# Kernel tuning notes

Hardware: AMD Instinct MI355X
Metric: run time of the kernel (lower is better)

## Reference

```python
import jax, jax.numpy as jnp
import numpy as np

H = 16        # heads
DH = 64       # dim_head
DM = 1024     # query_dim = context_dim
INNER = H * DH


def setup_inputs() -> dict:
    key = jax.random.key(0)
    ks = jax.random.split(key, 5)
    s = 0.02
    queries = jax.random.normal(ks[0], (2, 2048, DM), dtype=jnp.float32)
    Wq = jax.random.normal(ks[1], (DM, INNER), dtype=jnp.float32) * s
    Wkv = jax.random.normal(ks[2], (DM, 2 * INNER), dtype=jnp.float32) * s
    Wo = jax.random.normal(ks[3], (INNER, DM), dtype=jnp.float32) * s
    bo = jax.random.normal(ks[4], (DM,), dtype=jnp.float32) * s
    return {"queries": queries, "Wq": Wq, "Wkv": Wkv, "Wo": Wo, "bo": bo}


def reference(queries, Wq, Wkv, Wo, bo):
    b, n, _ = queries.shape
    scale = DH ** -0.5
    q = queries @ Wq                       # [b, n, inner]
    kv = queries @ Wkv                     # self-attention: context = queries
    k, v = jnp.split(kv, 2, axis=-1)
    # b n (h d) -> b h n d
    split_heads = lambda t: t.reshape(b, n, H, DH).transpose(0, 2, 1, 3)
    q, k, v = map(split_heads, (q, k, v))
    sim = jnp.einsum('bhid,bhjd->bhij', q, k) * scale
    attn = jax.nn.softmax(sim, axis=-1)    # dropout is identity (p=0 / eval)
    out = jnp.einsum('bhij,bhjd->bhid', attn, v)
    out = out.transpose(0, 2, 1, 3).reshape(b, n, INNER)
    return out @ Wo + bo
```

## Files before the change

### kernel.cpp

```cpp
#include <hip/hip_runtime.h>
#include <math.h>
#include <stdint.h>

typedef _Float16 half8v __attribute__((ext_vector_type(8)));
typedef _Float16 half4v __attribute__((ext_vector_type(4)));
typedef _Float16 half2v __attribute__((ext_vector_type(2)));
typedef __fp16 fp16x2 __attribute__((ext_vector_type(2)));
typedef float floatx4 __attribute__((ext_vector_type(4)));

#define MFMA16(a, b, c) __builtin_amdgcn_mfma_f32_16x16x32_f16(a, b, c, 0, 0, 0)

#define QSCALE 0.18033688011112f

__device__ __forceinline__ void gld_lds16(const void* g, void* l) {
  __builtin_amdgcn_global_load_lds(
      (const __attribute__((address_space(1))) uint32_t*)(uintptr_t)g,
      (__attribute__((address_space(3))) uint32_t*)(uintptr_t)l, 16, 0, 0);
}

__device__ __forceinline__ half2v pk16(float a, float b) {
  fp16x2 t = __builtin_amdgcn_cvt_pkrtz(a, b);
  return __builtin_bit_cast(half2v, t);
}

__device__ __forceinline__ int swz(int row, int blk) {
  return row * 64 + ((blk ^ (row & 7)) << 3);
}

__device__ __forceinline__ int vswz(int row, int blk) {
  return row * 32 + ((blk ^ ((row >> 1) & 3)) << 3);
}

__device__ __forceinline__ int gswz(int row, int blk) {
  return row * 32 + ((blk ^ ((row >> 1) & 3)) << 3);
}

__global__ __launch_bounds__(256) void prep(
    const float* __restrict__ X, const float* __restrict__ Wq,
    const float* __restrict__ Wkv, const float* __restrict__ Wo,
    _Float16* __restrict__ X16, _Float16* __restrict__ WqkvT,
    _Float16* __restrict__ WoT)
{
  __shared__ alignas(16) _Float16 Tt[64 * 68];
  const int bid = blockIdx.x;
  if (bid < 2048) {
    size_t gid = (size_t)bid * 256 + threadIdx.x;
    const float4* src = (const float4*)(X) + gid * 2;
    float4 a = src[0], b = src[1];
    half8v h;
    h[0]=(_Float16)a.x; h[1]=(_Float16)a.y; h[2]=(_Float16)a.z; h[3]=(_Float16)a.w;
    h[4]=(_Float16)b.x; h[5]=(_Float16)b.y; h[6]=(_Float16)b.z; h[7]=(_Float16)b.w;
    *((half8v*)X16 + gid) = h;
    return;
  }
  int b = bid - 2048;
  const float* src; _Float16* dst; int N, tk, tn;
  if (b < 256)      { src = Wq;  dst = WqkvT;                 N = 1024; tk = b & 15;        tn = b >> 4; }
  else if (b < 768) { src = Wkv; dst = WqkvT + (size_t)1024 * 1024; N = 2048; tk = (b - 256) & 15; tn = (b - 256) >> 4; }
  else              { src = Wo;  dst = WoT;                   N = 1024; tk = (b - 768) & 15; tn = (b - 768) >> 4; }

  const int t = threadIdx.x;
  {
    int kg = t >> 4, ng = t & 15;
    const float* sp = src + (size_t)(tk * 64 + kg * 4) * N + tn * 64 + ng * 4;
    float4 r0 = *(const float4*)(sp);
    float4 r1 = *(const float4*)(sp + N);
    float4 r2 = *(const float4*)(sp + 2 * N);
    float4 r3 = *(const float4*)(sp + 3 * N);
    half4v h;
    h[0]=(_Float16)r0.x; h[1]=(_Float16)r1.x; h[2]=(_Float16)r2.x; h[3]=(_Float16)r3.x;
    *(half4v*)&Tt[(ng * 4 + 0) * 68 + kg * 4] = h;
    h[0]=(_Float16)r0.y; h[1]=(_Float16)r1.y; h[2]=(_Float16)r2.y; h[3]=(_Float16)r3.y;
    *(half4v*)&Tt[(ng * 4 + 1) * 68 + kg * 4] = h;
    h[0]=(_Float16)r0.z; h[1]=(_Float16)r1.z; h[2]=(_Float16)r2.z; h[3]=(_Float16)r3.z;
    *(half4v*)&Tt[(ng * 4 + 2) * 68 + kg * 4] = h;
    h[0]=(_Float16)r0.w; h[1]=(_Float16)r1.w; h[2]=(_Float16)r2.w; h[3]=(_Float16)r3.w;
    *(half4v*)&Tt[(ng * 4 + 3) * 68 + kg * 4] = h;
  }
  __syncthreads();
  #pragma unroll
  for (int i = 0; i < 2; i++) {
    int idx = t + i * 256;
    int nl = idx >> 3, k8 = (idx & 7) * 8;
    half8v v = *(half8v*)&Tt[nl * 68 + k8];
    *(half8v*)(dst + (size_t)(tn * 64 + nl) * 1024 + tk * 64 + k8) = v;
  }
}

__global__ __launch_bounds__(256) void qkv_gemm(
    const _Float16* __restrict__ X16, const _Float16* __restrict__ WqkvT,
    _Float16* __restrict__ q_ws, _Float16* __restrict__ k_ws,
    _Float16* __restrict__ vT_ws)
{
  constexpr int K = 1024;
  __shared__ alignas(16) _Float16 Tt[128 * 136];
  _Float16* As = Tt;
  _Float16* Bs = Tt + 4096;

  const int m0 = blockIdx.x * 128;
  const int n0 = blockIdx.y * 128;

  const int tid  = threadIdx.x;
  const int wave = tid >> 6, lane = tid & 63;
  const int qd = lane >> 4, l15 = lane & 15;
  const int wr = (wave >> 1) * 64, wc = (wave & 1) * 64;
  const int r0i = tid >> 2;
  const int cbs = (((tid & 3) ^ ((r0i >> 1) & 3))) * 8;

  floatx4 acc[4][4] = {};

  for (int k0 = 0; k0 < K; k0 += 32) {
    gld_lds16(X16 + (size_t)(m0 + r0i) * K + k0 + cbs, &As[tid * 8]);
    gld_lds16(X16 + (size_t)(m0 + 64 + r0i) * K + k0 + cbs, &As[(tid + 256) * 8]);
    gld_lds16(WqkvT + (size_t)(n0 + r0i) * K + k0 + cbs, &Bs[tid * 8]);
    gld_lds16(WqkvT + (size_t)(n0 + 64 + r0i) * K + k0 + cbs, &Bs[(tid + 256) * 8]);
    __syncthreads();
    half8v a[4], b[4];
    #pragma unroll
    for (int it = 0; it < 4; it++)
      a[it] = *(half8v*)&As[gswz(wr + it * 16 + l15, qd)];
    #pragma unroll
    for (int jt = 0; jt < 4; jt++)
      b[jt] = *(half8v*)&Bs[gswz(wc + jt * 16 + l15, qd)];
    #pragma unroll
    for (int it = 0; it < 4; it++)
      #pragma unroll
      for (int jt = 0; jt < 4; jt++)
        acc[it][jt] = MFMA16(a[it], b[jt], acc[it][jt]);
    __syncthreads();
  }

  if (n0 < 2048) {
    #pragma unroll
    for (int it = 0; it < 4; it++) {
      #pragma unroll
      for (int jt = 0; jt < 4; jt++) {
        #pragma unroll
        for (int r = 0; r < 4; r++) {
          int m = m0 + wr + it * 16 + qd * 4 + r;
          int n = n0 + wc + jt * 16 + l15;
          float val = acc[it][jt][r];
          int bb = m >> 11, nn = m & 2047;
          if (n0 < 1024) {
            int h = n >> 6, d = n & 63;
            q_ws[(((size_t)bb * 16 + h) * 2048 + nn) * 64 + d] = (_Float16)(val * QSCALE);
          } else {
            int c = n - 1024, h = c >> 6, d = c & 63;
            k_ws[(((size_t)bb * 16 + h) * 2048 + nn) * 64 + d] = (_Float16)val;
          }
        }
      }
    }
  } else {
    #pragma unroll
    for (int it = 0; it < 4; it++) {
      #pragma unroll
      for (int jt = 0; jt < 4; jt++) {
        #pragma unroll
        for (int r = 0; r < 4; r++) {
          int ml = wr + it * 16 + qd * 4 + r;
          int nl = wc + jt * 16 + l15;
          Tt[nl * 136 + ml] = (_Float16)acc[it][jt][r];
        }
      }
    }
    __syncthreads();
    int row = tid >> 1;
    int mh  = (tid & 1) * 64;
    int c   = (n0 - 2048) + row;
    int bb  = m0 >> 11;
    int nnb = (m0 & 2047) + mh;
    _Float16* dstp =
        vT_ws + (((size_t)bb * 16 + (c >> 6)) * 64 + (c & 63)) * 2048 + nnb;
    #pragma unroll
    for (int i = 0; i < 8; i++)
      *(half8v*)(dstp + i * 8) = *(half8v*)&Tt[row * 136 + mh + i * 8];
  }
}

__global__ __launch_bounds__(256, 3) void attn_kernel(
    const _Float16* __restrict__ q_ws, const _Float16* __restrict__ k_ws,
    const _Float16* __restrict__ vT_ws, _Float16* __restrict__ aout)
{
  constexpr int N = 2048;
  __shared__ alignas(16) char smem[50176];
  _Float16* Kbase = (_Float16*)smem;
  _Float16* Vbase = (_Float16*)(smem + 16384);
  _Float16* PQ    = (_Float16*)(smem + 32768);

  const int id = blockIdx.x;
  const int bh = ((id >> 8) << 3) | (id & 7);
  const int qt = (id >> 3) & 31;

  const _Float16* Qp = q_ws + (size_t)bh * N * 64;
  const _Float16* Kp = k_ws + (size_t)bh * N * 64;
  const _Float16* Vp = vT_ws + (size_t)bh * 64 * N;

  const int tid = threadIdx.x, wave = tid >> 6, lane = tid & 63;
  const int qd = lane >> 4, l15 = lane & 15;
  const int q0 = qt * 64;
  const int wkv = wave * 32;

  _Float16* Ks = Kbase + wave * 2048;
  _Float16* Vs = Vbase + wave * 2048;
  _Float16* Ps = PQ + wave * 2048;

  const int krr = lane >> 3, kcb = (lane & 7) ^ krr;
  const int vrr = lane >> 2, vcb = (lane & 3) ^ ((lane >> 3) & 3);
  const int kwr = (krr * 64 + (kcb << 3));

  auto stage_v = [&](int il) {
    const _Float16* src = Vp + wkv + il * 128;
    #pragma unroll
    for (int j = 0; j < 4; j++)
      gld_lds16(src + (size_t)(j * 16 + vrr) * N + vcb * 8,
                Vs + (j * 64 + lane) * 8);
  };

  #pragma unroll
  for (int i = 0; i < 2; i++) {
    int idx = tid + i * 256;
    int r = idx >> 3, cb = (idx ^ r) & 7;
    gld_lds16(Qp + (size_t)(q0 + r) * 64 + cb * 8, PQ + idx * 8);
  }
  {
    const _Float16* src = Kp + (size_t)wkv * 64;
    #pragma unroll
    for (int j = 0; j < 4; j++)
      gld_lds16(src + (size_t)(j * 8 + krr) * 64 + kcb * 8,
                Ks + (j * 64 + lane) * 8);
  }
  stage_v(0);
  const _Float16* Kw = Kp + (size_t)wkv * 64;
  half8v kr0, kr1, kr2, kr3;
  {
    const _Float16* nb = Kw + (size_t)1 * 8192 + lane * 8;
    kr0 = *(const half8v*)(nb);
    kr1 = *(const half8v*)(nb + 512);
    kr2 = *(const half8v*)(nb + 1024);
    kr3 = *(const half8v*)(nb + 1536);
  }

  asm volatile("s_waitcnt vmcnt(8)" ::: "memory");
  __builtin_amdgcn_s_barrier();
  __builtin_amdgcn_sched_barrier(0);

  half8v qf[4][2];
  #pragma unroll
  for (int m = 0; m < 4; m++)
    #pragma unroll
    for (int ks = 0; ks < 2; ks++)
      qf[m][ks] = *(half8v*)&PQ[swz(m * 16 + l15, ks * 4 + qd)];

  asm volatile("s_waitcnt lgkmcnt(0)" ::: "memory");
  __builtin_amdgcn_s_barrier();
  __builtin_amdgcn_sched_barrier(0);

  floatx4 o[4][4] = {};
  float lsum[4] = {};

  for (int i = 0; i < 16; ++i) {
    floatx4 s[2][4] = {};
    #pragma unroll
    for (int ks = 0; ks < 2; ks++) {
      half8v kf0 = *(half8v*)&Ks[swz(l15, ks * 4 + qd)];
      half8v kf1 = *(half8v*)&Ks[swz(16 + l15, ks * 4 + qd)];
      __builtin_amdgcn_s_setprio(1);
      #pragma unroll
      for (int m = 0; m < 4; m++) {
        s[0][m] = MFMA16(kf0, qf[m][ks], s[0][m]);
        s[1][m] = MFMA16(kf1, qf[m][ks], s[1][m]);
      }
      __builtin_amdgcn_s_setprio(0);
    }

    #pragma unroll
    for (int m = 0; m < 4; m++)
      #pragma unroll
      for (int nt = 0; nt < 2; nt++) {
        float p0 = __builtin_amdgcn_exp2f(s[nt][m][0]);
        float p1 = __builtin_amdgcn_exp2f(s[nt][m][1]);
        float p2 = __builtin_amdgcn_exp2f(s[nt][m][2]);
        float p3 = __builtin_amdgcn_exp2f(s[nt][m][3]);
        lsum[m] += (p0 + p1) + (p2 + p3);
        half2v h01 = pk16(p0, p1);
        half2v h23 = pk16(p2, p3);
        half4v pk;
        pk[0] = h01[0]; pk[1] = h01[1]; pk[2] = h23[0]; pk[3] = h23[1];
        *(half4v*)&Ps[vswz(m * 16 + l15, 2 * nt + (qd >> 1)) + (qd & 1) * 4] = pk;
      }

    if (i < 15) asm volatile("s_waitcnt vmcnt(4)" ::: "memory");
    else        asm volatile("s_waitcnt vmcnt(0)" ::: "memory");
    __builtin_amdgcn_sched_barrier(0);

    half8v pf[4], vf[4];
    #pragma unroll
    for (int m = 0; m < 4; m++)
      pf[m] = *(half8v*)&Ps[vswz(m * 16 + l15, qd)];
    #pragma unroll
    for (int dt = 0; dt < 4; dt++)
      vf[dt] = *(half8v*)&Vs[vswz(dt * 16 + l15, qd)];

    asm volatile("s_waitcnt lgkmcnt(0)" ::: "memory");
    __builtin_amdgcn_sched_barrier(0);

    if (i < 15) {
      _Float16* wr = Ks + kwr;
      *(half8v*)(wr)        = kr0;
      *(half8v*)(wr + 512)  = kr1;
      *(half8v*)(wr + 1024) = kr2;
      *(half8v*)(wr + 1536) = kr3;
    }
    __builtin_amdgcn_sched_barrier(0);

    if (i < 15) stage_v(i + 1);
    if (i < 14) {
      const _Float16* nb = Kw + (size_t)(i + 2) * 8192 + lane * 8;
      kr0 = *(const half8v*)(nb);
      kr1 = *(const half8v*)(nb + 512);
      kr2 = *(const half8v*)(nb + 1024);
      kr3 = *(const half8v*)(nb + 1536);
    }
    __builtin_amdgcn_sched_barrier(0);

    __builtin_amdgcn_s_setprio(1);
    #pragma unroll
    for (int m = 0; m < 4; m++)
      #pragma unroll
      for (int dt = 0; dt < 4; dt++)
        o[m][dt] = MFMA16(pf[m], vf[dt], o[m][dt]);
    __builtin_amdgcn_s_setprio(0);
  }

  #pragma unroll
  for (int m = 0; m < 4; m++) {
    lsum[m] += __shfl_xor(lsum[m], 16);
    lsum[m] += __shfl_xor(lsum[m], 32);
  }

  __syncthreads();
  float* sc = (float*)smem;
  float* ls = (float*)(smem + 49152);
  #pragma unroll
  for (int m = 0; m < 4; m++)
    if (qd == 0) ls[wave * 64 + m * 16 + l15] = lsum[m];

  const int bb = bh >> 4, hh = bh & 15;
  #pragma unroll
  for (int pass = 0; pass < 2; pass++) {
    float* my = sc + wave * 2176;
    #pragma unroll
    for (int mm = 0; mm < 2; mm++) {
      int m = pass * 2 + mm;
      #pragma unroll
      for (int dt = 0; dt < 4; dt++)
        #pragma unroll
        for (int r = 0; r < 4; r++)
          my[(mm * 16 + qd * 4 + r) * 68 + dt * 16 + l15] = o[m][dt][r];
    }
    __syncthreads();
    {
      int r = tid >> 3, c0 = (tid & 7) * 8;
      int row = pass * 32 + r;
      float lsv = ls[row] + ls[64 + row] + ls[128 + row] + ls[192 + row];
      float inv = 1.0f / lsv;
      float acc8[8] = {};
      #pragma unroll
      for (int w = 0; w < 4; w++) {
        const float* p = sc + w * 2176 + r * 68 + c0;
        floatx4 a = *(const floatx4*)(p);
        floatx4 b = *(const floatx4*)(p + 4);
        acc8[0] += a[0]; acc8[1] += a[1]; acc8[2] += a[2]; acc8[3] += a[3];
        acc8[4] += b[0]; acc8[5] += b[1]; acc8[6] += b[2]; acc8[7] += b[3];
      }
      _Float16 hv[8];
      #pragma unroll
      for (int j = 0; j < 4; j++) {
        half2v h = pk16(acc8[2 * j] * inv, acc8[2 * j + 1] * inv);
        hv[2 * j] = h[0]; hv[2 * j + 1] = h[1];
      }
      _Float16* dst =
          aout + ((size_t)(bb * 2048 + q0 + row)) * 1024 + hh * 64 + c0;
      *(half8v*)dst = *(half8v*)hv;
    }
    if (pass == 0) __syncthreads();
  }
}

__global__ __launch_bounds__(256) void out_gemm(
    const _Float16* __restrict__ A, const _Float16* __restrict__ WoT,
    const float* __restrict__ bo, float* __restrict__ Out)
{
  constexpr int K = 1024;
  __shared__ alignas(16) _Float16 As[64 * 32];
  __shared__ alignas(16) _Float16 Bs[128 * 32];

  const int m0 = blockIdx.x * 64;
  const int n0 = blockIdx.y * 128;
  const int tid = threadIdx.x;
  const int wave = tid >> 6, lane = tid & 63;
  const int qd = lane >> 4, l15 = lane & 15;
  const int wr = (wave >> 1) * 32, wc = (wave & 1) * 64;
  const int r0i = tid >> 2;
  const int cbs = (((tid & 3) ^ ((r0i >> 1) & 3))) * 8;

  floatx4 acc[2][4] = {};

  for (int k0 = 0; k0 < K; k0 += 32) {
    gld_lds16(A + (size_t)(m0 + r0i) * K + k0 + cbs, &As[tid * 8]);
    gld_lds16(WoT + (size_t)(n0 + r0i) * K + k0 + cbs, &Bs[tid * 8]);
    gld_lds16(WoT + (size_t)(n0 + 64 + r0i) * K + k0 + cbs, &Bs[(tid + 256) * 8]);
    __syncthreads();
    half8v a[2], b[4];
    #pragma unroll
    for (int it = 0; it < 2; it++)
      a[it] = *(half8v*)&As[gswz(wr + it * 16 + l15, qd)];
    #pragma unroll
    for (int jt = 0; jt < 4; jt++)
      b[jt] = *(half8v*)&Bs[gswz(wc + jt * 16 + l15, qd)];
    #pragma unroll
    for (int it = 0; it < 2; it++)
      #pragma unroll
      for (int jt = 0; jt < 4; jt++)
        acc[it][jt] = MFMA16(a[it], b[jt], acc[it][jt]);
    __syncthreads();
  }

  #pragma unroll
  for (int it = 0; it < 2; it++) {
    #pragma unroll
    for (int jt = 0; jt < 4; jt++) {
      int n = n0 + wc + jt * 16 + l15;
      float bias = bo[n];
      #pragma unroll
      for (int r = 0; r < 4; r++) {
        int m = m0 + wr + it * 16 + qd * 4 + r;
        Out[(size_t)m * 1024 + n] = acc[it][jt][r] + bias;
      }
    }
  }
}

extern "C" void kernel_launch(void* const* d_in, const int* in_sizes, int n_in,
                              void* d_out, int out_size, void* d_ws, size_t ws_size,
                              hipStream_t stream) {
  const float* X   = (const float*)d_in[0];
  const float* Wq  = (const float*)d_in[1];
  const float* Wkv = (const float*)d_in[2];
  const float* Wo  = (const float*)d_in[3];
  const float* bo  = (const float*)d_in[4];
  float* out = (float*)d_out;

  const size_t M4 = (size_t)4 * 1024 * 1024;
  _Float16* q_ws   = (_Float16*)d_ws;
  _Float16* k_ws   = q_ws + M4;
  _Float16* vT_ws  = k_ws + M4;
  _Float16* X16    = vT_ws + M4;
  _Float16* WqkvT  = X16 + M4;
  _Float16* WoT    = WqkvT + (size_t)3 * 1024 * 1024;
  _Float16* aout   = X16;

  prep<<<3072, 256, 0, stream>>>(X, Wq, Wkv, Wo, X16, WqkvT, WoT);
  qkv_gemm<<<dim3(32, 24), 256, 0, stream>>>(X16, WqkvT, q_ws, k_ws, vT_ws);
  attn_kernel<<<1024, 256, 0, stream>>>(q_ws, k_ws, vT_ws, aout);
  out_gemm<<<dim3(64, 8), 256, 0, stream>>>(aout, WoT, bo, out);
}
```

Baseline: 201.9 us.

## Double GEMM K-tile depth, stream K via direct LDS loads, compute row sums with MFMA

Both projection GEMMs now stage a K-slab of 64 per iteration instead of 32, using an 8-block XOR swizzle. This halves the number of barrier pairs per tile and issues more MFMAs per sync. In attention, K tiles are prefetched with global-to-LDS async loads instead of being staged through registers and written back. Softmax row sums are also accumulated by an MFMA against a ones vector, which removes the per-element adds and cross-lane shuffles but adds extra MFMA work per iteration.

```diff
diff --git a/kernel.cpp b/kernel.cpp
--- a/kernel.cpp
+++ b/kernel.cpp
@@ -28,10 +28,6 @@
 }
 
 __device__ __forceinline__ int vswz(int row, int blk) {
-  return row * 32 + ((blk ^ ((row >> 1) & 3)) << 3);
-}
-
-__device__ __forceinline__ int gswz(int row, int blk) {
   return row * 32 + ((blk ^ ((row >> 1) & 3)) << 3);
 }
 
@@ -95,7 +91,7 @@
   constexpr int K = 1024;
   __shared__ alignas(16) _Float16 Tt[128 * 136];
   _Float16* As = Tt;
-  _Float16* Bs = Tt + 4096;
+  _Float16* Bs = Tt + 8192;
 
   const int m0 = blockIdx.x * 128;
   const int n0 = blockIdx.y * 128;
@@ -104,29 +100,38 @@
   const int wave = tid >> 6, lane = tid & 63;
   const int qd = lane >> 4, l15 = lane & 15;
   const int wr = (wave >> 1) * 64, wc = (wave & 1) * 64;
-  const int r0i = tid >> 2;
-  const int cbs = (((tid & 3) ^ ((r0i >> 1) & 3))) * 8;
 
   floatx4 acc[4][4] = {};
 
-  for (int k0 = 0; k0 < K; k0 += 32) {
-    gld_lds16(X16 + (size_t)(m0 + r0i) * K + k0 + cbs, &As[tid * 8]);
-    gld_lds16(X16 + (size_t)(m0 + 64 + r0i) * K + k0 + cbs, &As[(tid + 256) * 8]);
-    gld_lds16(WqkvT + (size_t)(n0 + r0i) * K + k0 + cbs, &Bs[tid * 8]);
-    gld_lds16(WqkvT + (size_t)(n0 + 64 + r0i) * K + k0 + cbs, &Bs[(tid + 256) * 8]);
-    __syncthreads();
-    half8v a[4], b[4];
-    #pragma unroll
-    for (int it = 0; it < 4; it++)
-      a[it] = *(half8v*)&As[gswz(wr + it * 16 + l15, qd)];
-    #pragma unroll
-    for (int jt = 0; jt < 4; jt++)
-      b[jt] = *(half8v*)&Bs[gswz(wc + jt * 16 + l15, qd)];
-    #pragma unroll
-    for (int it = 0; it < 4; it++)
+  for (int k0 = 0; k0 < K; k0 += 64) {
+    #pragma unroll
+    for (int i = 0; i < 4; i++) {
+      int idx = tid + i * 256;
+      int r = idx >> 3, cb = (idx ^ r) & 7;
+      gld_lds16(X16 + (size_t)(m0 + r) * K + k0 + cb * 8, &As[idx * 8]);
+    }
+    #pragma unroll
+    for (int i = 0; i < 4; i++) {
+      int idx = tid + i * 256;
+      int r = idx >> 3, cb = (idx ^ r) & 7;
+      gld_lds16(WqkvT + (size_t)(n0 + r) * K + k0 + cb * 8, &Bs[idx * 8]);
+    }
+    __syncthreads();
+    #pragma unroll
+    for (int ks = 0; ks < 2; ks++) {
+      half8v a[4], b[4];
+      #pragma unroll
+      for (int it = 0; it < 4; it++)
+        a[it] = *(half8v*)&As[swz(wr + it * 16 + l15, ks * 4 + qd)];
       #pragma unroll
       for (int jt = 0; jt < 4; jt++)
-        acc[it][jt] = MFMA16(a[it], b[jt], acc[it][jt]);
+        b[jt] = *(half8v*)&Bs[swz(wc + jt * 16 + l15, ks * 4 + qd)];
+      #pragma unroll
+      for (int it = 0; it < 4; it++)
+        #pragma unroll
+        for (int jt = 0; jt < 4; jt++)
+          acc[it][jt] = MFMA16(a[it], b[jt], acc[it][jt]);
+    }
     __syncthreads();
   }
 
@@ -207,8 +212,14 @@
 
   const int krr = lane >> 3, kcb = (lane & 7) ^ krr;
   const int vrr = lane >> 2, vcb = (lane & 3) ^ ((lane >> 3) & 3);
-  const int kwr = (krr * 64 + (kcb << 3));
-
+
+  auto stage_k = [&](int il) {
+    const _Float16* src = Kp + (size_t)(wkv + il * 128) * 64;
+    #pragma unroll
+    for (int j = 0; j < 4; j++)
+      gld_lds16(src + (size_t)(j * 8 + krr) * 64 + kcb * 8,
+                Ks + (j * 64 + lane) * 8);
+  };
   auto stage_v = [&](int il) {
     const _Float16* src = Vp + wkv + il * 128;
     #pragma unroll
@@ -223,23 +234,8 @@
     int r = idx >> 3, cb = (idx ^ r) & 7;
     gld_lds16(Qp + (size_t)(q0 + r) * 64 + cb * 8, PQ + idx * 8);
   }
-  {
-    const _Float16* src = Kp + (size_t)wkv * 64;
-    #pragma unroll
-    for (int j = 0; j < 4; j++)
-      gld_lds16(src + (size_t)(j * 8 + krr) * 64 + kcb * 8,
-                Ks + (j * 64 + lane) * 8);
-  }
+  stage_k(0);
   stage_v(0);
-  const _Float16* Kw = Kp + (size_t)wkv * 64;
-  half8v kr0, kr1, kr2, kr3;
-  {
-    const _Float16* nb = Kw + (size_t)1 * 8192 + lane * 8;
-    kr0 = *(const half8v*)(nb);
-    kr1 = *(const half8v*)(nb + 512);
-    kr2 = *(const half8v*)(nb + 1024);
-    kr3 = *(const half8v*)(nb + 1536);
-  }
 
   asm volatile("s_waitcnt vmcnt(8)" ::: "memory");
   __builtin_amdgcn_s_barrier();
@@ -256,23 +252,36 @@
   __builtin_amdgcn_s_barrier();
   __builtin_amdgcn_sched_barrier(0);
 
+  const half8v ones = {(_Float16)1, (_Float16)1, (_Float16)1, (_Float16)1,
+                       (_Float16)1, (_Float16)1, (_Float16)1, (_Float16)1};
   floatx4 o[4][4] = {};
-  float lsum[4] = {};
+  floatx4 ol[4] = {};
 
   for (int i = 0; i < 16; ++i) {
+    asm volatile("s_waitcnt vmcnt(4)" ::: "memory");
+    __builtin_amdgcn_sched_barrier(0);
+
+    half8v kf[2][2];
+    #pragma unroll
+    for (int ks = 0; ks < 2; ks++) {
+      kf[ks][0] = *(half8v*)&Ks[swz(l15, ks * 4 + qd)];
+      kf[ks][1] = *(half8v*)&Ks[swz(16 + l15, ks * 4 + qd)];
+    }
+    asm volatile("s_waitcnt lgkmcnt(0)" ::: "memory");
+    __builtin_amdgcn_sched_barrier(0);
+    if (i < 15) stage_k(i + 1);
+    __builtin_amdgcn_sched_barrier(0);
+
     floatx4 s[2][4] = {};
-    #pragma unroll
-    for (int ks = 0; ks < 2; ks++) {
-      half8v kf0 = *(half8v*)&Ks[swz(l15, ks * 4 + qd)];
-      half8v kf1 = *(half8v*)&Ks[swz(16 + l15, ks * 4 + qd)];
-      __builtin_amdgcn_s_setprio(1);
+    __builtin_amdgcn_s_setprio(1);
+    #pragma unroll
+    for (int ks = 0; ks < 2; ks++)
       #pragma unroll
       for (int m = 0; m < 4; m++) {
-        s[0][m] = MFMA16(kf0, qf[m][ks], s[0][m]);
-        s[1][m] = MFMA16(kf1, qf[m][ks], s[1][m]);
-      }
-      __builtin_amdgcn_s_setprio(0);
-    }
+        s[0][m] = MFMA16(kf[ks][0], qf[m][ks], s[0][m]);
+        s[1][m] = MFMA16(kf[ks][1], qf[m][ks], s[1][m]);
+      }
+    __builtin_amdgcn_s_setprio(0);
 
     #pragma unroll
     for (int m = 0; m < 4; m++)
@@ -282,7 +291,6 @@
         float p1 = __builtin_amdgcn_exp2f(s[nt][m][1]);
         float p2 = __builtin_amdgcn_exp2f(s[nt][m][2]);
         float p3 = __builtin_amdgcn_exp2f(s[nt][m][3]);
-        lsum[m] += (p0 + p1) + (p2 + p3);
         half2v h01 = pk16(p0, p1);
         half2v h23 = pk16(p2, p3);
         half4v pk;
@@ -294,49 +302,29 @@
     else        asm volatile("s_waitcnt vmcnt(0)" ::: "memory");
     __builtin_amdgcn_sched_barrier(0);
 
-    half8v pf[4], vf[4];
+    half8v pf[4], vfr[4];
     #pragma unroll
     for (int m = 0; m < 4; m++)
       pf[m] = *(half8v*)&Ps[vswz(m * 16 + l15, qd)];
     #pragma unroll
     for (int dt = 0; dt < 4; dt++)
-      vf[dt] = *(half8v*)&Vs[vswz(dt * 16 + l15, qd)];
+      vfr[dt] = *(half8v*)&Vs[vswz(dt * 16 + l15, qd)];
 
     asm volatile("s_waitcnt lgkmcnt(0)" ::: "memory");
     __builtin_amdgcn_sched_barrier(0);
-
-    if (i < 15) {
-      _Float16* wr = Ks + kwr;
-      *(half8v*)(wr)        = kr0;
-      *(half8v*)(wr + 512)  = kr1;
-      *(half8v*)(wr + 1024) = kr2;
-      *(half8v*)(wr + 1536) = kr3;
-    }
-    __builtin_amdgcn_sched_barrier(0);
-
     if (i < 15) stage_v(i + 1);
-    if (i < 14) {
-      const _Float16* nb = Kw + (size_t)(i + 2) * 8192 + lane * 8;
-      kr0 = *(const half8v*)(nb);
-      kr1 = *(const half8v*)(nb + 512);
-      kr2 = *(const half8v*)(nb + 1024);
-      kr3 = *(const half8v*)(nb + 1536);
-    }
     __builtin_amdgcn_sched_barrier(0);
 
     __builtin_amdgcn_s_setprio(1);
     #pragma unroll
     for (int m = 0; m < 4; m++)
+      ol[m] = MFMA16(pf[m], ones, ol[m]);
+    #pragma unroll
+    for (int m = 0; m < 4; m++)
       #pragma unroll
       for (int dt = 0; dt < 4; dt++)
-        o[m][dt] = MFMA16(pf[m], vf[dt], o[m][dt]);
+        o[m][dt] = MFMA16(pf[m], vfr[dt], o[m][dt]);
     __builtin_amdgcn_s_setprio(0);
-  }
-
-  #pragma unroll
-  for (int m = 0; m < 4; m++) {
-    lsum[m] += __shfl_xor(lsum[m], 16);
-    lsum[m] += __shfl_xor(lsum[m], 32);
   }
 
   __syncthreads();
@@ -344,7 +332,9 @@
   float* ls = (float*)(smem + 49152);
   #pragma unroll
   for (int m = 0; m < 4; m++)
-    if (qd == 0) ls[wave * 64 + m * 16 + l15] = lsum[m];
+    #pragma unroll
+    for (int r = 0; r < 4; r++)
+      ls[wave * 64 + m * 16 + qd * 4 + r] = ol[m][r];
 
   const int bb = bh >> 4, hh = bh & 15;
   #pragma unroll
@@ -393,8 +383,8 @@
     const float* __restrict__ bo, float* __restrict__ Out)
 {
   constexpr int K = 1024;
-  __shared__ alignas(16) _Float16 As[64 * 32];
-  __shared__ alignas(16) _Float16 Bs[128 * 32];
+  __shared__ alignas(16) _Float16 As[64 * 64];
+  __shared__ alignas(16) _Float16 Bs[128 * 64];
 
   const int m0 = blockIdx.x * 64;
   const int n0 = blockIdx.y * 128;
@@ -402,28 +392,41 @@
   const int wave = tid >> 6, lane = tid & 63;
   const int qd = lane >> 4, l15 = lane & 15;
   const int wr = (wave >> 1) * 32, wc = (wave & 1) * 64;
-  const int r0i = tid >> 2;
-  const int cbs = (((tid & 3) ^ ((r0i >> 1) & 3))) * 8;
 
   floatx4 acc[2][4] = {};
 
-  for (int k0 = 0; k0 < K; k0 += 32) {
-    gld_lds16(A + (size_t)(m0 + r0i) * K + k0 + cbs, &As[tid * 8]);
-    gld_lds16(WoT + (size_t)(n0 + r0i) * K + k0 + cbs, &Bs[tid * 8]);
-    gld_lds16(WoT + (size_t)(n0 + 64 + r0i) * K + k0 + cbs, &Bs[(tid + 256) * 8]);
-    __syncthreads();
-    half8v a[2], b[4];
+  for (int k0 = 0; k0 < K; k0 += 64) {
+    #pragma unroll
+    for (int i = 0; i < 2; i++) {
+      int idx = tid + i * 256;
+      int r = idx >> 3, cb = (idx ^ r) & 7;
+      gld_lds16(A + (size_t)(m0 + r) * K + k0 + cb * 8, &As[idx * 8]);
+    }
+    #pragma unroll
+    for (int i = 0; i < 4; i++) {
+      int idx = tid + i * 256;
+      int r = idx >> 3, cb = (idx ^ r) & 7;
+      gld_lds16(WoT + (size_t)(n0 + r) * K + k0 + cb * 8, &Bs[idx * 8]);
+    }
+    __syncthreads();
+    half8v a[2][2], b[4][2];
     #pragma unroll
     for (int it = 0; it < 2; it++)
-      a[it] = *(half8v*)&As[gswz(wr + it * 16 + l15, qd)];
+      #pragma unroll
+      for (int ks = 0; ks < 2; ks++)
+        a[it][ks] = *(half8v*)&As[swz(wr + it * 16 + l15, ks * 4 + qd)];
     #pragma unroll
     for (int jt = 0; jt < 4; jt++)
-      b[jt] = *(half8v*)&Bs[gswz(wc + jt * 16 + l15, qd)];
-    #pragma unroll
-    for (int it = 0; it < 2; it++)
-      #pragma unroll
-      for (int jt = 0; jt < 4; jt++)
-        acc[it][jt] = MFMA16(a[it], b[jt], acc[it][jt]);
+      #pragma unroll
+      for (int ks = 0; ks < 2; ks++)
+        b[jt][ks] = *(half8v*)&Bs[swz(wc + jt * 16 + l15, ks * 4 + qd)];
+    #pragma unroll
+    for (int ks = 0; ks < 2; ks++)
+      #pragma unroll
+      for (int it = 0; it < 2; it++)
+        #pragma unroll
+        for (int jt = 0; jt < 4; jt++)
+          acc[it][jt] = MFMA16(a[it][ks], b[jt][ks], acc[it][jt]);
     __syncthreads();
   }
 
```

New measurement: 200.2 us. Within noise of the previous version (-0.8%).
